# Performance work log

Hardware: AMD Instinct MI355X
Metric: run time of the kernel (lower is better)

The kernel has to match this reference:

```python
import jax, jax.numpy as jnp
import numpy as np

N = 32768      # total nodes (512 graphs x 64 padded nodes)
E = 262144     # edges (avg degree 8)
F_IN = 74      # atom feature dim
D0 = 128       # dim_embedding
D1 = 256       # hidden feats
B = 512        # batch_size (graphs)
NPG = 64       # nodes per graph
EPS = 1e-5     # BatchNorm1d eps


def setup_inputs() -> dict:
    key = jax.random.key(0)
    ks = jax.random.split(key, 8)
    def rn(k, shape, s=0.05):
        return jax.random.normal(k, shape, jnp.float32) * s
    # init_transform weight [D0, F_IN]; padding=True zeroes the last row
    W_init = rn(ks[0], (D0, F_IN)).at[-1].set(0.0)
    return {
        "node_feats": jax.random.normal(ks[1], (N, F_IN), jnp.float32),
        "W_init": W_init,
        "gcn_w1": rn(ks[2], (D0, D1)), "gcn_b1": jnp.zeros((D1,), jnp.float32),
        "res_w1": rn(ks[3], (D1, D0)), "res_b1": jnp.zeros((D1,), jnp.float32),
        "bn_g1": jnp.ones((D1,), jnp.float32), "bn_b1": jnp.zeros((D1,), jnp.float32),
        "gcn_w2": rn(ks[4], (D1, D1)), "gcn_b2": jnp.zeros((D1,), jnp.float32),
        "bn_g2": jnp.ones((D1,), jnp.float32), "bn_b2": jnp.zeros((D1,), jnp.float32),
        "edge_src": jax.random.randint(ks[5], (E,), 0, N),
        "edge_dst": jax.random.randint(ks[6], (E,), 0, N),
    }


def _agg(x, src, dst):
    # DGL GraphConv norm='both': D_out^{-1/2} gather-scatter D_in^{-1/2}, degrees clamped to >= 1
    ones = jnp.ones((src.shape[0],), x.dtype)
    deg_out = jnp.clip(jax.ops.segment_sum(ones, src, num_segments=N), 1.0)
    deg_in = jnp.clip(jax.ops.segment_sum(ones, dst, num_segments=N), 1.0)
    xs = x * jax.lax.rsqrt(deg_out)[:, None]
    agg = jax.ops.segment_sum(xs[src], dst, num_segments=N)  # [N, d]
    return agg * jax.lax.rsqrt(deg_in)[:, None]


def _bn(x, g, b):
    # BatchNorm1d training-mode: batch stats over node axis, biased var
    m = x.mean(0)
    v = x.var(0)
    return (x - m) * jax.lax.rsqrt(v + EPS) * g + b


def reference(node_feats, W_init, gcn_w1, gcn_b1, res_w1, res_b1, bn_g1, bn_b1,
              gcn_w2, gcn_b2, bn_g2, bn_b2, edge_src, edge_dst):
    h = node_feats @ W_init.T  # [N, D0]
    # layer 1: residual Linear 128->256, GCN(aggregate then weight, since in<out), GELU, BN
    res = h @ res_w1.T + res_b1
    g = jax.nn.gelu(_agg(h, edge_src, edge_dst) @ gcn_w1 + gcn_b1, approximate=False)
    h = _bn(g + res, bn_g1, bn_b1)
    # layer 2: Identity residual
    g = jax.nn.gelu(_agg(h, edge_src, edge_dst) @ gcn_w2 + gcn_b2, approximate=False)
    h = _bn(g + h, bn_g2, bn_b2)
    return h.reshape(B, NPG, D1)
```

## Files before the change

### kernel.cpp

```cpp
#include <hip/hip_runtime.h>
#include <hip/hip_bf16.h>
#include <math.h>

#define N_NODES 32768
#define E_EDGES 262144
#define F_INF   74
#define KP      96
#define D0      128
#define D1      256
#define BN_EPS  1e-5f
#define RBLK    1024

typedef float f32x4 __attribute__((ext_vector_type(4)));
typedef short s16x8 __attribute__((ext_vector_type(8)));

__device__ __forceinline__ float b2f(ushort h) { return __uint_as_float(((unsigned)h) << 16); }
__device__ __forceinline__ ushort f2b(float f) {
    unsigned u = __float_as_uint(f);
    return (ushort)((u + 0x7FFFu + ((u >> 16) & 1u)) >> 16);
}
__device__ __forceinline__ unsigned char f2q(float f) {
    unsigned u = __float_as_uint(f * 7.52316384526264005e-37f);
    unsigned s = (u >> 24) & 0x80u;
    int r = (int)(((u & 0x7fffffffu) + 0x80000u) >> 20);
    r = r > 126 ? 126 : r;
    return (unsigned char)(s | (unsigned)r);
}
__device__ __forceinline__ float q2f(unsigned x) {
    unsigned fb = ((x & 0x80u) << 24) | ((x & 0x7fu) << 20);
    return __uint_as_float(fb) * 1.32922799578491587e+36f;
}
__device__ __forceinline__ void acc_q(float* a, uint4 q, float c) {
    unsigned d;
    d = q.x; a[0]  += q2f(d & 255u) * c; a[1]  += q2f((d >> 8) & 255u) * c;
             a[2]  += q2f((d >> 16) & 255u) * c; a[3]  += q2f(d >> 24) * c;
    d = q.y; a[4]  += q2f(d & 255u) * c; a[5]  += q2f((d >> 8) & 255u) * c;
             a[6]  += q2f((d >> 16) & 255u) * c; a[7]  += q2f(d >> 24) * c;
    d = q.z; a[8]  += q2f(d & 255u) * c; a[9]  += q2f((d >> 8) & 255u) * c;
             a[10] += q2f((d >> 16) & 255u) * c; a[11] += q2f(d >> 24) * c;
    d = q.w; a[12] += q2f(d & 255u) * c; a[13] += q2f((d >> 8) & 255u) * c;
             a[14] += q2f((d >> 16) & 255u) * c; a[15] += q2f(d >> 24) * c;
}
__device__ __forceinline__ float gelu_exact(float x) {
    return 0.5f * x * (1.0f + erff(x * 0.70710678118654752440f));
}


__global__ void k_front_a(const int* __restrict__ src, const int* __restrict__ dst,
                          int* __restrict__ deg,
                          const float* __restrict__ nf, const float* __restrict__ Wi,
                          const float* __restrict__ w1, const float* __restrict__ rw,
                          const float* __restrict__ w2,
                          ushort* __restrict__ nfB, ushort* __restrict__ WTB,
                          ushort* __restrict__ WB1, ushort* __restrict__ RWB,
                          ushort* __restrict__ WB2) {
    int bid = blockIdx.x;
    int tid = threadIdx.x;
    if (bid < 1024) {
        int e = bid * 256 + tid;
        atomicAdd(&deg[src[e]], 1);
        atomicAdd(&deg[N_NODES + dst[e]], 1);
        return;
    }
    int idx = (bid - 1024) * 256 + tid;
    {
        int n = idx / KP, k = idx - n * KP;
        nfB[idx] = (k < F_INF) ? f2b(nf[n * F_INF + k]) : (ushort)0;
    }
    if (idx < D0 * KP) {
        int c = idx / KP, k = idx - c * KP;
        WTB[idx] = (k < F_INF) ? f2b(Wi[c * F_INF + k]) : (ushort)0;
    }
    if (idx < D1 * D0) {
        int n = idx >> 7, k = idx & 127;
        WB1[idx] = f2b(w1[k * D1 + n]);
        RWB[idx] = f2b(rw[idx]);
    }
    if (idx < D1 * D1) {
        int n = idx >> 8, k = idx & 255;
        WB2[idx] = f2b(w2[k * D1 + n]);
    }
}

__global__ __launch_bounds__(1024) void k_scan(const int* __restrict__ deg,
                                               int* __restrict__ row_off,
                                               float* __restrict__ rsq_out,
                                               float* __restrict__ rsq_in,
                                               int* __restrict__ cursor) {
    __shared__ int part[1024];
    int t = threadIdx.x;
    int base = t * 32;
    int loc[32];
    int s = 0;
    #pragma unroll
    for (int i = 0; i < 32; i++) { loc[i] = s; s += deg[N_NODES + base + i]; }
    part[t] = s;
    #pragma unroll
    for (int i = 0; i < 32; i++) {
        int n = base + i;
        int d_o = deg[n];           if (d_o < 1) d_o = 1;
        int d_i = deg[N_NODES + n]; if (d_i < 1) d_i = 1;
        rsq_out[n] = 1.0f / sqrtf((float)d_o);
        rsq_in[n]  = 1.0f / sqrtf((float)d_i);
        cursor[n] = 0;
    }
    __syncthreads();
    for (int off = 1; off < 1024; off <<= 1) {
        int v = 0;
        if (t >= off) v = part[t - off];
        __syncthreads();
        if (t >= off) part[t] += v;
        __syncthreads();
    }
    int pre = (t == 0) ? 0 : part[t - 1];
    #pragma unroll
    for (int i = 0; i < 32; i++) row_off[base + i] = pre + loc[i];
    if (t == 1023) row_off[N_NODES] = part[1023];
}


__global__ __launch_bounds__(512) void k_front_b(
    const int* __restrict__ src, const int* __restrict__ dst,
    const int* __restrict__ row_off, const float* __restrict__ rsq_out,
    int* __restrict__ cursor, int* __restrict__ csr_src, float* __restrict__ esc,
    const ushort* __restrict__ nfB, const ushort* __restrict__ WTB,
    ushort* __restrict__ h0) {
    int bid = blockIdx.x;
    int tid = threadIdx.x;
    if (bid < 512) {
        int e = bid * 512 + tid;
        int d = dst[e];
        int s = src[e];
        int slot = atomicAdd(&cursor[d], 1);
        int pos = row_off[d] + slot;
        csr_src[pos] = s;
        esc[pos] = rsq_out[s];
        return;
    }
    int b2 = bid - 512;
    int w = tid >> 6, lane = tid & 63, m = lane & 15, g4 = lane >> 4;
    int col = w * 16 + m;
    int rbase = b2 * 16;
    s16x8 B[3], A[3];
    #pragma unroll
    for (int j = 0; j < 3; j++)
        B[j] = *reinterpret_cast<const s16x8*>(&WTB[(size_t)col * KP + j * 32 + g4 * 8]);
    #pragma unroll
    for (int j = 0; j < 3; j++)
        A[j] = *reinterpret_cast<const s16x8*>(&nfB[(size_t)(rbase + m) * KP + j * 32 + g4 * 8]);
    f32x4 acc = (f32x4){0.f, 0.f, 0.f, 0.f};
    #pragma unroll
    for (int j = 0; j < 3; j++)
        acc = __builtin_amdgcn_mfma_f32_16x16x32_bf16(A[j], B[j], acc, 0, 0, 0);
    #pragma unroll
    for (int r = 0; r < 4; r++)
        h0[(size_t)(rbase + g4 * 4 + r) * D0 + col] = f2b(acc[r]);
}


__global__ __launch_bounds__(512) void k_layer1f(
    const ushort* __restrict__ h0B, const float* __restrict__ rsq_in,
    const int* __restrict__ row_off, const int* __restrict__ csr_src,
    const float* __restrict__ esc,
    const ushort* __restrict__ WB1, const ushort* __restrict__ RWB,
    const float* __restrict__ b1, const float* __restrict__ rb,
    ushort* __restrict__ t1B, unsigned char* __restrict__ t1Q,
    float* __restrict__ partials) {
    __shared__ ushort sA[32 * 128];
    int tid = threadIdx.x;
    int rbase = blockIdx.x * 32;
    {
        int nloc = tid >> 4;
        int node = rbase + nloc;
        int f = (tid & 15) * 8;
        int beg = row_off[node], end = row_off[node + 1];
        float a[8];
        #pragma unroll
        for (int j = 0; j < 8; j++) a[j] = 0.f;
        int e = beg;
        for (; e + 3 < end; e += 4) {
            int s0 = csr_src[e], s1 = csr_src[e + 1], s2 = csr_src[e + 2], s3 = csr_src[e + 3];
            float c0 = esc[e], c1 = esc[e + 1], c2 = esc[e + 2], c3 = esc[e + 3];
            s16x8 v0 = *reinterpret_cast<const s16x8*>(&h0B[(size_t)s0 * D0 + f]);
            s16x8 v1 = *reinterpret_cast<const s16x8*>(&h0B[(size_t)s1 * D0 + f]);
            s16x8 v2 = *reinterpret_cast<const s16x8*>(&h0B[(size_t)s2 * D0 + f]);
            s16x8 v3 = *reinterpret_cast<const s16x8*>(&h0B[(size_t)s3 * D0 + f]);
            #pragma unroll
            for (int j = 0; j < 8; j++)
                a[j] += b2f((ushort)v0[j]) * c0 + b2f((ushort)v1[j]) * c1 +
                        b2f((ushort)v2[j]) * c2 + b2f((ushort)v3[j]) * c3;
        }
        for (; e < end; e++) {
            int s = csr_src[e];
            float sc = esc[e];
            s16x8 v = *reinterpret_cast<const s16x8*>(&h0B[(size_t)s * D0 + f]);
            #pragma unroll
            for (int j = 0; j < 8; j++) a[j] += b2f((ushort)v[j]) * sc;
        }
        float si = rsq_in[node];
        s16x8 o;
        #pragma unroll
        for (int j = 0; j < 8; j++) o[j] = (short)f2b(a[j] * si);
        int boff = nloc * 256 + ((f * 2) ^ ((nloc & 15) << 4));
        *reinterpret_cast<s16x8*>(((char*)sA) + boff) = o;
    }
    __syncthreads();
    int w = tid >> 6, lane = tid & 63, m = lane & 15, g4 = lane >> 4;
    int cb = w * 32;
    s16x8 BG[2][4], BR[2][4];
    #pragma unroll
    for (int nt = 0; nt < 2; nt++)
        #pragma unroll
        for (int j = 0; j < 4; j++) {
            BG[nt][j] = *reinterpret_cast<const s16x8*>(&WB1[(size_t)(cb + nt * 16 + m) * D0 + j * 32 + g4 * 8]);
            BR[nt][j] = *reinterpret_cast<const s16x8*>(&RWB[(size_t)(cb + nt * 16 + m) * D0 + j * 32 + g4 * 8]);
        }
    float bg[2], brv[2];
    #pragma unroll
    for (int nt = 0; nt < 2; nt++) {
        bg[nt]  = b1[cb + nt * 16 + m];
        brv[nt] = rb[cb + nt * 16 + m];
    }
    float ps[2] = {0.f, 0.f}, pq[2] = {0.f, 0.f};
    #pragma unroll
    for (int rt = 0; rt < 2; rt++) {
        int row = rt * 16 + m;
        s16x8 aA[4], aH[4];
        #pragma unroll
        for (int j = 0; j < 4; j++) {
            int boff = row * 256 + (((j * 4 + g4) * 16) ^ ((row & 15) << 4));
            aA[j] = *reinterpret_cast<const s16x8*>(((const char*)sA) + boff);
            aH[j] = *reinterpret_cast<const s16x8*>(&h0B[(size_t)(rbase + row) * D0 + j * 32 + g4 * 8]);
        }
        f32x4 accG[2], accR[2];
        #pragma unroll
        for (int nt = 0; nt < 2; nt++) {
            accG[nt] = (f32x4){0.f, 0.f, 0.f, 0.f};
            accR[nt] = (f32x4){0.f, 0.f, 0.f, 0.f};
        }
        #pragma unroll
        for (int j = 0; j < 4; j++)
            #pragma unroll
            for (int nt = 0; nt < 2; nt++) {
                accG[nt] = __builtin_amdgcn_mfma_f32_16x16x32_bf16(aA[j], BG[nt][j], accG[nt], 0, 0, 0);
                accR[nt] = __builtin_amdgcn_mfma_f32_16x16x32_bf16(aH[j], BR[nt][j], accR[nt], 0, 0, 0);
            }
        #pragma unroll
        for (int nt = 0; nt < 2; nt++) {
            int col = cb + nt * 16 + m;
            #pragma unroll
            for (int r = 0; r < 4; r++) {
                int orow = rbase + rt * 16 + g4 * 4 + r;
                float v = gelu_exact(accG[nt][r] + bg[nt]) + accR[nt][r] + brv[nt];
                t1B[(size_t)orow * D1 + col] = f2b(v);
                t1Q[(size_t)orow * D1 + col] = f2q(v);
                ps[nt] += v; pq[nt] += v * v;
            }
        }
    }
    #pragma unroll
    for (int nt = 0; nt < 2; nt++) {
        float s = ps[nt], q = pq[nt];
        s += __shfl_xor(s, 16); s += __shfl_xor(s, 32);
        q += __shfl_xor(q, 16); q += __shfl_xor(q, 32);
        if (g4 == 0) {
            int col = cb + nt * 16 + m;
            partials[(size_t)col * RBLK + blockIdx.x] = s;
            partials[(size_t)(256 + col) * RBLK + blockIdx.x] = q;
        }
    }
}


__global__ __launch_bounds__(1024) void k_layer2f(
    const ushort* __restrict__ t1B, const unsigned char* __restrict__ t1Q,
    const float* __restrict__ sc1, const float* __restrict__ sh1,
    const float* __restrict__ rsq_in,
    const int* __restrict__ row_off, const int* __restrict__ csr_src,
    const float* __restrict__ esc,
    const ushort* __restrict__ WB2, const float* __restrict__ b2,
    ushort* __restrict__ t2B, float* __restrict__ partials) {
    __shared__ ushort sA[32 * 256];
    int tid = threadIdx.x;
    int rbase = blockIdx.x * 32;
    {
        int nloc = tid >> 5;
        int half = (tid >> 4) & 1;
        int node = rbase + nloc;
        int f0 = (tid & 15) * 16;
        int beg = row_off[node], end = row_off[node + 1];
        float a[16];
        #pragma unroll
        for (int j = 0; j < 16; j++) a[j] = 0.f;
        float ssum = 0.f;
        int e = beg + half;
        for (; e + 6 < end; e += 8) {
            int s0 = csr_src[e], s1 = csr_src[e + 2], s2 = csr_src[e + 4], s3 = csr_src[e + 6];
            float c0 = esc[e], c1 = esc[e + 2], c2 = esc[e + 4], c3 = esc[e + 6];
            uint4 q0 = *reinterpret_cast<const uint4*>(&t1Q[(size_t)s0 * D1 + f0]);
            uint4 q1 = *reinterpret_cast<const uint4*>(&t1Q[(size_t)s1 * D1 + f0]);
            uint4 q2 = *reinterpret_cast<const uint4*>(&t1Q[(size_t)s2 * D1 + f0]);
            uint4 q3 = *reinterpret_cast<const uint4*>(&t1Q[(size_t)s3 * D1 + f0]);
            ssum += c0 + c1 + c2 + c3;
            acc_q(a, q0, c0); acc_q(a, q1, c1); acc_q(a, q2, c2); acc_q(a, q3, c3);
        }
        for (; e < end; e += 2) {
            int s = csr_src[e];
            float sc = esc[e];
            uint4 q = *reinterpret_cast<const uint4*>(&t1Q[(size_t)s * D1 + f0]);
            ssum += sc;
            acc_q(a, q, sc);
        }
        #pragma unroll
        for (int j = 0; j < 16; j++) a[j] += __shfl_xor(a[j], 16);
        ssum += __shfl_xor(ssum, 16);
        if (half == 0) {
            float si = rsq_in[node];
            s16x8 o0, o1;
            #pragma unroll
            for (int j = 0; j < 8; j++) {
                o0[j] = (short)f2b((sc1[f0 + j] * a[j] + sh1[f0 + j] * ssum) * si);
                o1[j] = (short)f2b((sc1[f0 + 8 + j] * a[8 + j] + sh1[f0 + 8 + j] * ssum) * si);
            }
            int swz = (nloc & 15) << 4;
            int x0 = f0 * 2;
            *reinterpret_cast<s16x8*>(((char*)sA) + nloc * 512 + (x0 ^ swz)) = o0;
            *reinterpret_cast<s16x8*>(((char*)sA) + nloc * 512 + ((x0 + 16) ^ swz)) = o1;
        }
    }
    __syncthreads();
    int w = tid >> 6, lane = tid & 63, m = lane & 15, g4 = lane >> 4;
    int col = w * 16 + m;
    ushort rres[2][4];
    #pragma unroll
    for (int rt = 0; rt < 2; rt++)
        #pragma unroll
        for (int r = 0; r < 4; r++)
            rres[rt][r] = t1B[(size_t)(rbase + rt * 16 + g4 * 4 + r) * D1 + col];
    s16x8 BG[8];
    #pragma unroll
    for (int j = 0; j < 8; j++)
        BG[j] = *reinterpret_cast<const s16x8*>(&WB2[(size_t)col * D1 + j * 32 + g4 * 8]);
    float bg = b2[col], a1c = sc1[col], s1c = sh1[col];
    float ps = 0.f, pq = 0.f;
    #pragma unroll
    for (int rt = 0; rt < 2; rt++) {
        int row = rt * 16 + m;
        s16x8 aA[8];
        #pragma unroll
        for (int j = 0; j < 8; j++) {
            int boff = row * 512 + (((j * 4 + g4) * 16) ^ ((row & 15) << 4));
            aA[j] = *reinterpret_cast<const s16x8*>(((const char*)sA) + boff);
        }
        f32x4 acc = (f32x4){0.f, 0.f, 0.f, 0.f};
        #pragma unroll
        for (int j = 0; j < 8; j++)
            acc = __builtin_amdgcn_mfma_f32_16x16x32_bf16(aA[j], BG[j], acc, 0, 0, 0);
        #pragma unroll
        for (int r = 0; r < 4; r++) {
            int orow = rbase + rt * 16 + g4 * 4 + r;
            float h1v = fmaf(b2f(rres[rt][r]), a1c, s1c);
            float v = gelu_exact(acc[r] + bg) + h1v;
            t2B[(size_t)orow * D1 + col] = f2b(v);
            ps += v; pq += v * v;
        }
    }
    ps += __shfl_xor(ps, 16); ps += __shfl_xor(ps, 32);
    pq += __shfl_xor(pq, 16); pq += __shfl_xor(pq, 32);
    if (g4 == 0) {
        partials[(size_t)col * RBLK + blockIdx.x] = ps;
        partials[(size_t)(256 + col) * RBLK + blockIdx.x] = pq;
    }
}


__global__ __launch_bounds__(256) void k_reduce(
    const float* __restrict__ partials, const float* __restrict__ g,
    const float* __restrict__ b, float* __restrict__ sc, float* __restrict__ sh) {
    int c = blockIdx.x;
    int t = threadIdx.x;
    const float* ps = partials + (size_t)c * RBLK;
    const float* pq = partials + (size_t)(256 + c) * RBLK;
    float s = ps[t] + ps[t + 256] + ps[t + 512] + ps[t + 768];
    float q = pq[t] + pq[t + 256] + pq[t + 512] + pq[t + 768];
    __shared__ float Ls[256], Lq[256];
    Ls[t] = s; Lq[t] = q;
    __syncthreads();
    for (int o = 128; o > 0; o >>= 1) {
        if (t < o) { Ls[t] += Ls[t + o]; Lq[t] += Lq[t + o]; }
        __syncthreads();
    }
    if (t == 0) {
        float m = Ls[0] * (1.0f / (float)N_NODES);
        float var = Lq[0] * (1.0f / (float)N_NODES) - m * m;
        float a = g[c] / sqrtf(var + BN_EPS);
        sc[c] = a;
        sh[c] = b[c] - m * a;
    }
}


__global__ __launch_bounds__(256) void k_apply(
    const ushort* __restrict__ t2B, const float* __restrict__ sc,
    const float* __restrict__ sh, float* __restrict__ out) {
    int idx = blockIdx.x * 256 + threadIdx.x;
    size_t base = (size_t)idx * 8;
    int c = (int)(base & 255);
    s16x8 v = *reinterpret_cast<const s16x8*>(&t2B[base]);
    float4 o0, o1;
    o0.x = fmaf(b2f((ushort)v[0]), sc[c + 0], sh[c + 0]);
    o0.y = fmaf(b2f((ushort)v[1]), sc[c + 1], sh[c + 1]);
    o0.z = fmaf(b2f((ushort)v[2]), sc[c + 2], sh[c + 2]);
    o0.w = fmaf(b2f((ushort)v[3]), sc[c + 3], sh[c + 3]);
    o1.x = fmaf(b2f((ushort)v[4]), sc[c + 4], sh[c + 4]);
    o1.y = fmaf(b2f((ushort)v[5]), sc[c + 5], sh[c + 5]);
    o1.z = fmaf(b2f((ushort)v[6]), sc[c + 6], sh[c + 6]);
    o1.w = fmaf(b2f((ushort)v[7]), sc[c + 7], sh[c + 7]);
    *reinterpret_cast<float4*>(&out[base]) = o0;
    *reinterpret_cast<float4*>(&out[base + 4]) = o1;
}


static inline size_t align256(size_t x) { return (x + 255) & ~(size_t)255; }

extern "C" void kernel_launch(void* const* d_in, const int* in_sizes, int n_in,
                              void* d_out, int out_size, void* d_ws, size_t ws_size,
                              hipStream_t stream) {
    const float* node_feats = (const float*)d_in[0];
    const float* W_init     = (const float*)d_in[1];
    const float* gcn_w1     = (const float*)d_in[2];
    const float* gcn_b1     = (const float*)d_in[3];
    const float* res_w1     = (const float*)d_in[4];
    const float* res_b1     = (const float*)d_in[5];
    const float* bn_g1      = (const float*)d_in[6];
    const float* bn_b1      = (const float*)d_in[7];
    const float* gcn_w2     = (const float*)d_in[8];
    const float* gcn_b2     = (const float*)d_in[9];
    const float* bn_g2      = (const float*)d_in[10];
    const float* bn_b2      = (const float*)d_in[11];
    const int*   edge_src   = (const int*)d_in[12];
    const int*   edge_dst   = (const int*)d_in[13];
    float* out = (float*)d_out;

    char* p = (char*)d_ws;
    size_t off = 0;
    auto take = [&](size_t bytes) { void* r = p + off; off += align256(bytes); return r; };

    ushort* h0B   = (ushort*)take((size_t)N_NODES * D0 * 2);
    ushort* t1B   = (ushort*)take((size_t)N_NODES * D1 * 2);
    unsigned char* t1Q = (unsigned char*)take((size_t)N_NODES * D1);
    ushort* t2B   = (ushort*)take((size_t)N_NODES * D1 * 2);
    ushort* nfB   = (ushort*)take((size_t)N_NODES * KP * 2);
    ushort* WTB   = (ushort*)take((size_t)D0 * KP * 2);
    ushort* WB1   = (ushort*)take((size_t)D1 * D0 * 2);
    ushort* RWB   = (ushort*)take((size_t)D1 * D0 * 2);
    ushort* WB2   = (ushort*)take((size_t)D1 * D1 * 2);
    float*  part1 = (float*)take((size_t)2 * 256 * RBLK * 4);
    float*  part2 = (float*)take((size_t)2 * 256 * RBLK * 4);
    float*  sc1   = (float*)take(256 * 4);
    float*  sh1   = (float*)take(256 * 4);
    float*  sc2   = (float*)take(256 * 4);
    float*  sh2   = (float*)take(256 * 4);
    float*  rsq_out = (float*)take((size_t)N_NODES * 4);
    float*  rsq_in  = (float*)take((size_t)N_NODES * 4);
    int*    degi    = (int*)take((size_t)2 * N_NODES * 4);
    int*    cursor  = (int*)take((size_t)N_NODES * 4);
    int*    row_off = (int*)take((size_t)(N_NODES + 2) * 4);
    int*    csr_src = (int*)take((size_t)E_EDGES * 4);
    float*  esc     = (float*)take((size_t)E_EDGES * 4);

    hipMemsetAsync(degi, 0, (size_t)2 * N_NODES * 4, stream);

    k_front_a<<<1024 + (N_NODES * KP) / 256, 256, 0, stream>>>(
        edge_src, edge_dst, degi, node_feats, W_init, gcn_w1, res_w1, gcn_w2,
        nfB, WTB, WB1, RWB, WB2);

    k_scan<<<1, 1024, 0, stream>>>(degi, row_off, rsq_out, rsq_in, cursor);

    k_front_b<<<512 + N_NODES / 16, 512, 0, stream>>>(
        edge_src, edge_dst, row_off, rsq_out, cursor, csr_src, esc, nfB, WTB, h0B);

    k_layer1f<<<RBLK, 512, 0, stream>>>(h0B, rsq_in, row_off, csr_src, esc,
                                        WB1, RWB, gcn_b1, res_b1, t1B, t1Q, part1);
    k_reduce<<<256, 256, 0, stream>>>(part1, bn_g1, bn_b1, sc1, sh1);

    k_layer2f<<<RBLK, 1024, 0, stream>>>(t1B, t1Q, sc1, sh1, rsq_in, row_off, csr_src, esc,
                                         WB2, gcn_b2, t2B, part2);
    k_reduce<<<256, 256, 0, stream>>>(part2, bn_g2, bn_b2, sc2, sh2);

    k_apply<<<(N_NODES * D1 / 8) / 256, 256, 0, stream>>>(t2B, sc2, sh2, out);
}
```

Measured before the change: 216.5 us.

## Gather layer-1 features in 8-bit format and use hardware FP8 conversion

The front kernel now writes an extra 8-bit quantized copy of h0. The layer-1 neighbour gather reads this copy instead of the bf16 one, which halves the bytes fetched per edge. The dequantization helper uses the hardware packed FP8-to-float conversion when that builtin is available, and the layer-2 gather is split into two 8-byte column chunks to match. The risks are extra precision loss in layer 1, a mismatch between the custom q2f encoding and the hardware FP8 format, and an additional store in the front kernel.

```diff
diff --git a/kernel.cpp b/kernel.cpp
--- a/kernel.cpp
+++ b/kernel.cpp
@@ -11,7 +11,14 @@
 #define BN_EPS  1e-5f
 #define RBLK    1024
 
+#if __has_builtin(__builtin_amdgcn_cvt_pk_f32_fp8)
+#define HW_FP8 1
+#else
+#define HW_FP8 0
+#endif
+
 typedef float f32x4 __attribute__((ext_vector_type(4)));
+typedef float f32x2 __attribute__((ext_vector_type(2)));
 typedef short s16x8 __attribute__((ext_vector_type(8)));
 
 __device__ __forceinline__ float b2f(ushort h) { return __uint_as_float(((unsigned)h) << 16); }
@@ -30,16 +37,20 @@
     unsigned fb = ((x & 0x80u) << 24) | ((x & 0x7fu) << 20);
     return __uint_as_float(fb) * 1.32922799578491587e+36f;
 }
-__device__ __forceinline__ void acc_q(float* a, uint4 q, float c) {
+__device__ __forceinline__ void acc8(float* a, uint2 v, float c) {
+#if HW_FP8
+    f32x2 p;
+    p = __builtin_amdgcn_cvt_pk_f32_fp8((int)v.x, false); a[0] += p[0] * c; a[1] += p[1] * c;
+    p = __builtin_amdgcn_cvt_pk_f32_fp8((int)v.x, true);  a[2] += p[0] * c; a[3] += p[1] * c;
+    p = __builtin_amdgcn_cvt_pk_f32_fp8((int)v.y, false); a[4] += p[0] * c; a[5] += p[1] * c;
+    p = __builtin_amdgcn_cvt_pk_f32_fp8((int)v.y, true);  a[6] += p[0] * c; a[7] += p[1] * c;
+#else
     unsigned d;
-    d = q.x; a[0]  += q2f(d & 255u) * c; a[1]  += q2f((d >> 8) & 255u) * c;
-             a[2]  += q2f((d >> 16) & 255u) * c; a[3]  += q2f(d >> 24) * c;
-    d = q.y; a[4]  += q2f(d & 255u) * c; a[5]  += q2f((d >> 8) & 255u) * c;
-             a[6]  += q2f((d >> 16) & 255u) * c; a[7]  += q2f(d >> 24) * c;
-    d = q.z; a[8]  += q2f(d & 255u) * c; a[9]  += q2f((d >> 8) & 255u) * c;
-             a[10] += q2f((d >> 16) & 255u) * c; a[11] += q2f(d >> 24) * c;
-    d = q.w; a[12] += q2f(d & 255u) * c; a[13] += q2f((d >> 8) & 255u) * c;
-             a[14] += q2f((d >> 16) & 255u) * c; a[15] += q2f(d >> 24) * c;
+    d = v.x; a[0] += q2f(d & 255u) * c; a[1] += q2f((d >> 8) & 255u) * c;
+             a[2] += q2f((d >> 16) & 255u) * c; a[3] += q2f(d >> 24) * c;
+    d = v.y; a[4] += q2f(d & 255u) * c; a[5] += q2f((d >> 8) & 255u) * c;
+             a[6] += q2f((d >> 16) & 255u) * c; a[7] += q2f(d >> 24) * c;
+#endif
 }
 __device__ __forceinline__ float gelu_exact(float x) {
     return 0.5f * x * (1.0f + erff(x * 0.70710678118654752440f));
@@ -124,7 +135,7 @@
     const int* __restrict__ row_off, const float* __restrict__ rsq_out,
     int* __restrict__ cursor, int* __restrict__ csr_src, float* __restrict__ esc,
     const ushort* __restrict__ nfB, const ushort* __restrict__ WTB,
-    ushort* __restrict__ h0) {
+    ushort* __restrict__ h0, unsigned char* __restrict__ h0Q) {
     int bid = blockIdx.x;
     int tid = threadIdx.x;
     if (bid < 512) {
@@ -153,13 +164,16 @@
     for (int j = 0; j < 3; j++)
         acc = __builtin_amdgcn_mfma_f32_16x16x32_bf16(A[j], B[j], acc, 0, 0, 0);
     #pragma unroll
-    for (int r = 0; r < 4; r++)
+    for (int r = 0; r < 4; r++) {
         h0[(size_t)(rbase + g4 * 4 + r) * D0 + col] = f2b(acc[r]);
+        h0Q[(size_t)(rbase + g4 * 4 + r) * D0 + col] = f2q(acc[r]);
+    }
 }
 
 
 __global__ __launch_bounds__(512) void k_layer1f(
-    const ushort* __restrict__ h0B, const float* __restrict__ rsq_in,
+    const ushort* __restrict__ h0B, const unsigned char* __restrict__ h0Q,
+    const float* __restrict__ rsq_in,
     const int* __restrict__ row_off, const int* __restrict__ csr_src,
     const float* __restrict__ esc,
     const ushort* __restrict__ WB1, const ushort* __restrict__ RWB,
@@ -181,21 +195,17 @@
         for (; e + 3 < end; e += 4) {
             int s0 = csr_src[e], s1 = csr_src[e + 1], s2 = csr_src[e + 2], s3 = csr_src[e + 3];
             float c0 = esc[e], c1 = esc[e + 1], c2 = esc[e + 2], c3 = esc[e + 3];
-            s16x8 v0 = *reinterpret_cast<const s16x8*>(&h0B[(size_t)s0 * D0 + f]);
-            s16x8 v1 = *reinterpret_cast<const s16x8*>(&h0B[(size_t)s1 * D0 + f]);
-            s16x8 v2 = *reinterpret_cast<const s16x8*>(&h0B[(size_t)s2 * D0 + f]);
-            s16x8 v3 = *reinterpret_cast<const s16x8*>(&h0B[(size_t)s3 * D0 + f]);
-            #pragma unroll
-            for (int j = 0; j < 8; j++)
-                a[j] += b2f((ushort)v0[j]) * c0 + b2f((ushort)v1[j]) * c1 +
-                        b2f((ushort)v2[j]) * c2 + b2f((ushort)v3[j]) * c3;
+            uint2 q0 = *reinterpret_cast<const uint2*>(&h0Q[(size_t)s0 * D0 + f]);
+            uint2 q1 = *reinterpret_cast<const uint2*>(&h0Q[(size_t)s1 * D0 + f]);
+            uint2 q2 = *reinterpret_cast<const uint2*>(&h0Q[(size_t)s2 * D0 + f]);
+            uint2 q3 = *reinterpret_cast<const uint2*>(&h0Q[(size_t)s3 * D0 + f]);
+            acc8(a, q0, c0); acc8(a, q1, c1); acc8(a, q2, c2); acc8(a, q3, c3);
         }
         for (; e < end; e++) {
             int s = csr_src[e];
             float sc = esc[e];
-            s16x8 v = *reinterpret_cast<const s16x8*>(&h0B[(size_t)s * D0 + f]);
-            #pragma unroll
-            for (int j = 0; j < 8; j++) a[j] += b2f((ushort)v[j]) * sc;
+            uint2 q = *reinterpret_cast<const uint2*>(&h0Q[(size_t)s * D0 + f]);
+            acc8(a, q, sc);
         }
         float si = rsq_in[node];
         s16x8 o;
@@ -287,45 +297,57 @@
         int nloc = tid >> 5;
         int half = (tid >> 4) & 1;
         int node = rbase + nloc;
-        int f0 = (tid & 15) * 16;
+        int f0 = (tid & 15) * 8;
         int beg = row_off[node], end = row_off[node + 1];
-        float a[16];
-        #pragma unroll
-        for (int j = 0; j < 16; j++) a[j] = 0.f;
+        float a0[8], a1[8];
+        #pragma unroll
+        for (int j = 0; j < 8; j++) { a0[j] = 0.f; a1[j] = 0.f; }
         float ssum = 0.f;
         int e = beg + half;
         for (; e + 6 < end; e += 8) {
             int s0 = csr_src[e], s1 = csr_src[e + 2], s2 = csr_src[e + 4], s3 = csr_src[e + 6];
             float c0 = esc[e], c1 = esc[e + 2], c2 = esc[e + 4], c3 = esc[e + 6];
-            uint4 q0 = *reinterpret_cast<const uint4*>(&t1Q[(size_t)s0 * D1 + f0]);
-            uint4 q1 = *reinterpret_cast<const uint4*>(&t1Q[(size_t)s1 * D1 + f0]);
-            uint4 q2 = *reinterpret_cast<const uint4*>(&t1Q[(size_t)s2 * D1 + f0]);
-            uint4 q3 = *reinterpret_cast<const uint4*>(&t1Q[(size_t)s3 * D1 + f0]);
+            uint2 qa0 = *reinterpret_cast<const uint2*>(&t1Q[(size_t)s0 * D1 + f0]);
+            uint2 qb0 = *reinterpret_cast<const uint2*>(&t1Q[(size_t)s0 * D1 + f0 + 128]);
+            uint2 qa1 = *reinterpret_cast<const uint2*>(&t1Q[(size_t)s1 * D1 + f0]);
+            uint2 qb1 = *reinterpret_cast<const uint2*>(&t1Q[(size_t)s1 * D1 + f0 + 128]);
+            uint2 qa2 = *reinterpret_cast<const uint2*>(&t1Q[(size_t)s2 * D1 + f0]);
+            uint2 qb2 = *reinterpret_cast<const uint2*>(&t1Q[(size_t)s2 * D1 + f0 + 128]);
+            uint2 qa3 = *reinterpret_cast<const uint2*>(&t1Q[(size_t)s3 * D1 + f0]);
+            uint2 qb3 = *reinterpret_cast<const uint2*>(&t1Q[(size_t)s3 * D1 + f0 + 128]);
             ssum += c0 + c1 + c2 + c3;
-            acc_q(a, q0, c0); acc_q(a, q1, c1); acc_q(a, q2, c2); acc_q(a, q3, c3);
+            acc8(a0, qa0, c0); acc8(a1, qb0, c0);
+            acc8(a0, qa1, c1); acc8(a1, qb1, c1);
+            acc8(a0, qa2, c2); acc8(a1, qb2, c2);
+            acc8(a0, qa3, c3); acc8(a1, qb3, c3);
         }
         for (; e < end; e += 2) {
             int s = csr_src[e];
             float sc = esc[e];
-            uint4 q = *reinterpret_cast<const uint4*>(&t1Q[(size_t)s * D1 + f0]);
+            uint2 qa = *reinterpret_cast<const uint2*>(&t1Q[(size_t)s * D1 + f0]);
+            uint2 qb = *reinterpret_cast<const uint2*>(&t1Q[(size_t)s * D1 + f0 + 128]);
             ssum += sc;
-            acc_q(a, q, sc);
-        }
-        #pragma unroll
-        for (int j = 0; j < 16; j++) a[j] += __shfl_xor(a[j], 16);
+            acc8(a0, qa, sc); acc8(a1, qb, sc);
+        }
+        #pragma unroll
+        for (int j = 0; j < 8; j++) {
+            a0[j] += __shfl_xor(a0[j], 16);
+            a1[j] += __shfl_xor(a1[j], 16);
+        }
         ssum += __shfl_xor(ssum, 16);
         if (half == 0) {
             float si = rsq_in[node];
             s16x8 o0, o1;
             #pragma unroll
             for (int j = 0; j < 8; j++) {
-                o0[j] = (short)f2b((sc1[f0 + j] * a[j] + sh1[f0 + j] * ssum) * si);
-                o1[j] = (short)f2b((sc1[f0 + 8 + j] * a[8 + j] + sh1[f0 + 8 + j] * ssum) * si);
+                o0[j] = (short)f2b((sc1[f0 + j] * a0[j] + sh1[f0 + j] * ssum) * si);
+                o1[j] = (short)f2b((sc1[f0 + 128 + j] * a1[j] + sh1[f0 + 128 + j] * ssum) * si);
             }
             int swz = (nloc & 15) << 4;
-            int x0 = f0 * 2;
-            *reinterpret_cast<s16x8*>(((char*)sA) + nloc * 512 + (x0 ^ swz)) = o0;
-            *reinterpret_cast<s16x8*>(((char*)sA) + nloc * 512 + ((x0 + 16) ^ swz)) = o1;
+            int b0 = nloc * 512 + ((f0 * 2) ^ swz);
+            int b1_ = nloc * 512 + (((f0 + 128) * 2) ^ swz);
+            *reinterpret_cast<s16x8*>(((char*)sA) + b0) = o0;
+            *reinterpret_cast<s16x8*>(((char*)sA) + b1_) = o1;
         }
     }
     __syncthreads();
@@ -447,6 +469,7 @@
     auto take = [&](size_t bytes) { void* r = p + off; off += align256(bytes); return r; };
 
     ushort* h0B   = (ushort*)take((size_t)N_NODES * D0 * 2);
+    unsigned char* h0Q = (unsigned char*)take((size_t)N_NODES * D0);
     ushort* t1B   = (ushort*)take((size_t)N_NODES * D1 * 2);
     unsigned char* t1Q = (unsigned char*)take((size_t)N_NODES * D1);
     ushort* t2B   = (ushort*)take((size_t)N_NODES * D1 * 2);
@@ -478,9 +501,9 @@
     k_scan<<<1, 1024, 0, stream>>>(degi, row_off, rsq_out, rsq_in, cursor);
 
     k_front_b<<<512 + N_NODES / 16, 512, 0, stream>>>(
-        edge_src, edge_dst, row_off, rsq_out, cursor, csr_src, esc, nfB, WTB, h0B);
-
-    k_layer1f<<<RBLK, 512, 0, stream>>>(h0B, rsq_in, row_off, csr_src, esc,
+        edge_src, edge_dst, row_off, rsq_out, cursor, csr_src, esc, nfB, WTB, h0B, h0Q);
+
+    k_layer1f<<<RBLK, 512, 0, stream>>>(h0B, h0Q, rsq_in, row_off, csr_src, esc,
                                         WB1, RWB, gcn_b1, res_b1, t1B, t1Q, part1);
     k_reduce<<<256, 256, 0, stream>>>(part1, bn_g1, bn_b1, sc1, sh1);
 
```

Result: faster. 203.2 us (-6.1%).
